# Kernel optimization log

Hardware: AMD Instinct MI355X
Metric: run time of the kernel (lower is better)

The kernel has to match this reference:

```python
import jax, jax.numpy as jnp
import numpy as np

B, T, C, H = 1, 4096, 768, 12
D = C // H  # 64


def setup_inputs() -> dict:
    key = jax.random.key(0)
    k1, k2, k3, k4, k5 = jax.random.split(key, 5)
    x = jax.random.normal(k1, (B, T, C), dtype=jnp.float32)
    # causal mask: 1.0 where attention is DISALLOWED (strict upper triangle)
    mask = (1.0 - jnp.tril(jnp.ones((T, T), dtype=jnp.float32)))[None, None, :, :]
    s_attn = 1.0 / np.sqrt(C)
    W_qkv = jax.random.normal(k2, (C, 3 * C), dtype=jnp.float32) * s_attn
    b_qkv = jnp.zeros((3 * C,), dtype=jnp.float32)
    W_proj = jax.random.normal(k3, (C, C), dtype=jnp.float32) * s_attn
    b_proj = jnp.zeros((C,), dtype=jnp.float32)
    return {"x": x, "mask": mask, "W_qkv": W_qkv, "b_qkv": b_qkv,
            "W_proj": W_proj, "b_proj": b_proj}


def reference(x, mask, W_qkv, b_qkv, W_proj, b_proj):
    qkv = jnp.einsum('btc,cf->btf', x, W_qkv) + b_qkv        # [B,T,3C]
    q, k, v = jnp.split(qkv, 3, axis=2)
    # [B,T,C] -> [B,H,T,D]
    q = q.reshape(B, T, H, D).transpose(0, 2, 1, 3)
    k = k.reshape(B, T, H, D).transpose(0, 2, 1, 3)
    v = v.reshape(B, T, H, D).transpose(0, 2, 1, 3)
    att = jnp.einsum('bhqd,bhkd->bhqk', q, k) * (1.0 / jnp.sqrt(jnp.float32(D)))
    att = att + mask * (-1e9)
    att = jax.nn.softmax(att, axis=-1)                        # [B,H,T,T]
    y = jnp.einsum('bhqk,bhkd->bhqd', att, v)                 # [B,H,T,D]
    y = y.transpose(0, 2, 1, 3).reshape(B, T, C)
    return jnp.einsum('btc,cf->btf', y, W_proj) + b_proj
```

## Files before the change

kernel.cpp:

```cpp
#include <hip/hip_runtime.h>
#include <hip/hip_bf16.h>

typedef unsigned short u16t;
typedef short bf16x8 __attribute__((ext_vector_type(8)));
typedef short bf16x4 __attribute__((ext_vector_type(4)));
typedef float f32x4 __attribute__((ext_vector_type(4)));

#define T_SEQ 4096
#define NH    12
#define HD    64
#define C3    2304
#define CDIM  768
#define STRIP_KV 512
#define SLOTS 144
#define SC_F  0.18033688011112042f

__device__ __forceinline__ float bf2f(u16t u) {
  union { unsigned int i; float f; } c; c.i = ((unsigned int)u) << 16; return c.f;
}
__device__ __forceinline__ u16t f2bf(float f) {
  union { float f; unsigned int i; } c; c.f = f;
  unsigned int u = c.i;
  u += 0x7fffu + ((u >> 16) & 1u);
  return (u16t)(u >> 16);
}
__device__ __forceinline__ unsigned pk2bf(float a, float b) {
  __hip_bfloat162 h = __float22bfloat162_rn(make_float2(a, b));
  union { __hip_bfloat162 h; unsigned u; } c; c.h = h; return c.u;
}
__device__ __forceinline__ void gload16(const u16t* g, u16t* l) {
  __builtin_amdgcn_global_load_lds((const __attribute__((address_space(1))) void*)g,
                                   (__attribute__((address_space(3))) void*)l,
                                   16, 0, 0);
}

#define BARRIER_LGKM() __asm__ __volatile__("s_waitcnt lgkmcnt(0)\n\ts_barrier" ::: "memory")

__global__ __launch_bounds__(256) void convert_to_bf16(const float* __restrict__ in,
                                                       u16t* __restrict__ out, int n) {
  int i = blockIdx.x * 256 + threadIdx.x;
  const int stride = gridDim.x * 256;
  for (; i < n; i += stride) out[i] = f2bf(in[i]);
}

__global__ __launch_bounds__(256) void transpose_weights(const float* __restrict__ Wqkv,
                                                         const float* __restrict__ Wproj,
                                                         u16t* __restrict__ WqkvT,
                                                         u16t* __restrict__ WprojT) {
  __shared__ u16t tile[32][33];
  const int z = blockIdx.z;
  const int Cc = z ? CDIM : C3;
  if (z && blockIdx.x >= (unsigned)(CDIM / 32)) return;
  const float* in = z ? Wproj : Wqkv;
  u16t* out = z ? WprojT : WqkvT;
  const int tx = threadIdx.x, ty = threadIdx.y;
  const int c0 = blockIdx.x * 32, r0 = blockIdx.y * 32;
#pragma unroll
  for (int i = 0; i < 32; i += 8)
    tile[ty + i][tx] = f2bf(in[(size_t)(r0 + ty + i) * Cc + c0 + tx]);
  __syncthreads();
#pragma unroll
  for (int i = 0; i < 32; i += 8)
    out[(size_t)(c0 + ty + i) * CDIM + r0 + tx] = tile[tx][ty + i];
}

template <int MT, int NF, bool OUTF32>
__global__ __launch_bounds__(256) void gemm_bt_bias(
    const u16t* __restrict__ A, const u16t* __restrict__ Bt,
    const float* __restrict__ bias, void* __restrict__ Cout,
    int M, int N, int K, int qcols, float qscale) {
  constexpr int BN = 32 * NF;
  constexpr int MI = MT / 32;
  __shared__ u16t lA[2][MT * 32];
  __shared__ u16t lB[2][BN * 32];
  const int t = threadIdx.x;
  const int lane = t & 63;
  const int wid  = t >> 6;
  const int quad = lane >> 4, l16 = lane & 15;
  const int m0 = blockIdx.y * MT, n0 = blockIdx.x * BN;
  const int wm = (wid >> 1) * (16 * MI), wn = (wid & 1) * (16 * NF);

  f32x4 acc[MI][NF];
#pragma unroll
  for (int i = 0; i < MI; ++i)
#pragma unroll
    for (int j = 0; j < NF; ++j) acc[i][j] = (f32x4){0.f, 0.f, 0.f, 0.f};

  for (int k0 = 0; k0 < K; k0 += 64) {
#pragma unroll
    for (int half = 0; half < 2; ++half) {
      const int kk = k0 + half * 32;
#pragma unroll
      for (int rd = 0; rd < MT / 64; ++rd) {
        const int e = rd * 256 + t;
        gload16(A + (size_t)(m0 + (e >> 2)) * K + kk + (e & 3) * 8, &lA[half][e * 8]);
      }
#pragma unroll
      for (int rd = 0; rd < NF / 2; ++rd) {
        const int e = rd * 256 + t;
        gload16(Bt + (size_t)(n0 + (e >> 2)) * K + kk + (e & 3) * 8, &lB[half][e * 8]);
      }
    }
    __syncthreads();
#pragma unroll
    for (int half = 0; half < 2; ++half) {
      bf16x8 af[MI], bfr[NF];
#pragma unroll
      for (int i = 0; i < MI; ++i)
        af[i] = *(const bf16x8*)&lA[half][(wm + i * 16 + l16) * 32 + quad * 8];
#pragma unroll
      for (int i = 0; i < NF; ++i)
        bfr[i] = *(const bf16x8*)&lB[half][(wn + i * 16 + l16) * 32 + quad * 8];
#pragma unroll
      for (int i = 0; i < MI; ++i)
#pragma unroll
        for (int j = 0; j < NF; ++j)
          acc[i][j] = __builtin_amdgcn_mfma_f32_16x16x32_bf16(af[i], bfr[j], acc[i][j], 0, 0, 0);
    }
    __syncthreads();
  }

#pragma unroll
  for (int j = 0; j < NF; ++j) {
    const int col = n0 + wn + j * 16 + l16;
    const float bv = bias[col];
    const float cs = (col < qcols) ? qscale : 1.0f;
#pragma unroll
    for (int i = 0; i < MI; ++i) {
      const int rowb = m0 + wm + i * 16 + quad * 4;
#pragma unroll
      for (int r = 0; r < 4; ++r) {
        const float val = (acc[i][j][r] + bv) * cs;
        const size_t idx = (size_t)(rowb + r) * N + col;
        if (OUTF32) ((float*)Cout)[idx] = val;
        else        ((u16t*)Cout)[idx] = f2bf(val);
      }
    }
  }
}

#define KSTR 88
#define VSTR 88

__global__ __launch_bounds__(256, 4) void attn_partial(const u16t* __restrict__ qkv,
                                                       u16t* __restrict__ pO,
                                                       float* __restrict__ pL) {
  const int h     = blockIdx.x;
  const int strip = blockIdx.y;
  const int qt    = 31 - (int)blockIdx.z;
  const int q0 = qt * 128;
  const int kv_begin = strip * STRIP_KV;
  const int kv_end   = q0 + 128;
  if (kv_begin >= kv_end) return;
  const int kv_stop = (kv_begin + STRIP_KV < kv_end) ? kv_begin + STRIP_KV : kv_end;
  const int a = qt >> 2, b = qt & 3;
  const int slot = (a + 1) * (2 * a + b) + strip;

  __shared__ u16t lK[64 * KSTR];
  __shared__ u16t lVt[64 * VSTR];

  const int t = threadIdx.x;
  const int lane = t & 63;
  const int wid  = t >> 6;
  const int quad = lane >> 4, l16 = lane & 15;
  const int wr = q0 + wid * 32;

  const int krow = t >> 3, kcol = (t & 7) * 8;
  const int vk0 = 4 * (t >> 4);
  const int vd0 = 4 * (t & 15);
  const int vswz = (t & 3) << 3;
  const u16t* Kbase = qkv + CDIM + h * HD;
  const u16t* Vbase = qkv + 2 * CDIM + h * HD;

  bf16x8 qf[2][2];
#pragma unroll
  for (int qn = 0; qn < 2; ++qn) {
    const int row = wr + qn * 16 + l16;
#pragma unroll
    for (int kd = 0; kd < 2; ++kd)
      qf[qn][kd] = *(const bf16x8*)(qkv + (size_t)row * C3 + h * HD + kd * 32 + quad * 8);
  }

  f32x4 oaccT[4][2];
  f32x4 laccT[2];
#pragma unroll
  for (int dn = 0; dn < 4; ++dn)
#pragma unroll
    for (int qn = 0; qn < 2; ++qn) oaccT[dn][qn] = (f32x4){0.f, 0.f, 0.f, 0.f};
#pragma unroll
  for (int qn = 0; qn < 2; ++qn) laccT[qn] = (f32x4){0.f, 0.f, 0.f, 0.f};
  bf16x4 ones4;
#pragma unroll
  for (int i = 0; i < 4; ++i) ones4[i] = (short)0x3F80;

  const int pswz = ((l16 >> 2) & 3) << 3;

  uint4 kreg0, kreg1;
  union { uint2 u; u16t hw[4]; } vreg[4];

#define LOAD_TILE(KV0)                                                        \
  do {                                                                        \
    kreg0 = *(const uint4*)(Kbase + (size_t)((KV0) + krow) * C3 + kcol);      \
    kreg1 = *(const uint4*)(Kbase + (size_t)((KV0) + krow + 32) * C3 + kcol); \
    _Pragma("unroll")                                                         \
    for (int i = 0; i < 4; ++i)                                               \
      vreg[i].u = *(const uint2*)(Vbase + (size_t)((KV0) + vk0 + i) * C3 + vd0); \
  } while (0)

#define STORE_TILE()                                                          \
  do {                                                                        \
    *(uint4*)&lK[krow * KSTR + kcol] = kreg0;                                 \
    *(uint4*)&lK[(krow + 32) * KSTR + kcol] = kreg1;                          \
    _Pragma("unroll")                                                         \
    for (int j = 0; j < 4; ++j) {                                             \
      union { uint2 u; u16t hw[4]; } w;                                       \
      w.hw[0] = vreg[0].hw[j]; w.hw[1] = vreg[1].hw[j];                       \
      w.hw[2] = vreg[2].hw[j]; w.hw[3] = vreg[3].hw[j];                       \
      *(uint2*)&lVt[(vd0 + j) * VSTR + (vk0 ^ vswz)] = w.u;                   \
    }                                                                         \
  } while (0)

  LOAD_TILE(kv_begin);
  STORE_TILE();

  for (int kv0 = kv_begin; kv0 < kv_stop; kv0 += 64) {
    const bool havenext = (kv0 + 64 < kv_stop);
    if (havenext) LOAD_TILE(kv0 + 64);
    BARRIER_LGKM();

    if (kv0 <= wr + 31) {
      f32x4 sacc[4][2];
#pragma unroll
      for (int kvt = 0; kvt < 4; ++kvt) {
        bf16x8 kf0 = *(const bf16x8*)&lK[(kvt * 16 + l16) * KSTR + quad * 8];
        bf16x8 kf1 = *(const bf16x8*)&lK[(kvt * 16 + l16) * KSTR + 32 + quad * 8];
#pragma unroll
        for (int qn = 0; qn < 2; ++qn) {
          f32x4 s = (f32x4){0.f, 0.f, 0.f, 0.f};
          s = __builtin_amdgcn_mfma_f32_16x16x32_bf16(kf0, qf[qn][0], s, 0, 0, 0);
          s = __builtin_amdgcn_mfma_f32_16x16x32_bf16(kf1, qf[qn][1], s, 0, 0, 0);
          sacc[kvt][qn] = s;
        }
      }
      const bool need_mask = (kv0 + 63 > wr);
      bf16x4 pbf[4][2];
#pragma unroll
      for (int kvt = 0; kvt < 4; ++kvt)
#pragma unroll
        for (int qn = 0; qn < 2; ++qn) {
          const int qg = wr + qn * 16 + l16;
          float pv[4];
#pragma unroll
          for (int r = 0; r < 4; ++r) {
            const int kvg = kv0 + kvt * 16 + quad * 4 + r;
            float p = __builtin_amdgcn_exp2f(sacc[kvt][qn][r]);
            if (need_mask && (kvg > qg)) p = 0.f;
            pv[r] = p;
          }
          union { bf16x4 v; unsigned u[2]; } pw;
          pw.u[0] = pk2bf(pv[0], pv[1]);
          pw.u[1] = pk2bf(pv[2], pv[3]);
          pbf[kvt][qn] = pw.v;
        }
#pragma unroll
      for (int kvt = 0; kvt < 4; ++kvt) {
        const int kvcol = (kvt * 16 + quad * 4) ^ pswz;
#pragma unroll
        for (int qn = 0; qn < 2; ++qn)
          laccT[qn] = __builtin_amdgcn_mfma_f32_16x16x16bf16_1k(
              ones4, pbf[kvt][qn], laccT[qn], 0, 0, 0);
#pragma unroll
        for (int dn = 0; dn < 4; ++dn) {
          bf16x4 vf = *(const bf16x4*)&lVt[(dn * 16 + l16) * VSTR + kvcol];
#pragma unroll
          for (int qn = 0; qn < 2; ++qn)
            oaccT[dn][qn] = __builtin_amdgcn_mfma_f32_16x16x16bf16_1k(
                vf, pbf[kvt][qn], oaccT[dn][qn], 0, 0, 0);
        }
      }
    }
    BARRIER_LGKM();
    if (havenext) STORE_TILE();
  }

  {
    u16t* scr = &lVt[wid * 16 * 80];
    u16t* po = pO + ((size_t)h * SLOTS + slot) * 128 * HD;
    float* pl = pL + ((size_t)h * SLOTS + slot) * 128;
#pragma unroll
    for (int qn = 0; qn < 2; ++qn) {
#pragma unroll
      for (int dn = 0; dn < 4; ++dn) {
        union { bf16x4 v; unsigned u[2]; } w;
        w.u[0] = pk2bf(oaccT[dn][qn][0], oaccT[dn][qn][1]);
        w.u[1] = pk2bf(oaccT[dn][qn][2], oaccT[dn][qn][3]);
        *(bf16x4*)&scr[l16 * 80 + dn * 16 + quad * 4] = w.v;
      }
      __asm__ __volatile__("s_waitcnt lgkmcnt(0)" ::: "memory");
      const int ql = wid * 32 + qn * 16 + l16;
      uint4 w0 = *(const uint4*)&scr[l16 * 80 + quad * 16];
      uint4 w1 = *(const uint4*)&scr[l16 * 80 + quad * 16 + 8];
      u16t* dst = po + (size_t)ql * HD + quad * 16;
      *(uint4*)dst = w0;
      *(uint4*)(dst + 8) = w1;
      if (quad == 0) pl[ql] = laccT[qn][0];
      __asm__ __volatile__("s_waitcnt lgkmcnt(0)" ::: "memory");
    }
  }
#undef LOAD_TILE
#undef STORE_TILE
}

__global__ __launch_bounds__(256) void attn_normalize(const u16t* __restrict__ pO,
                                                      const float* __restrict__ pL,
                                                      u16t* __restrict__ y) {
  const int i = blockIdx.x * 256 + threadIdx.x;
  const int q = i / (CDIM / 8), c8 = (i % (CDIM / 8)) * 8;
  const int h = c8 >> 6, d = c8 & 63;
  const int qt = q >> 7, ql = q & 127;
  const int a = qt >> 2, b = qt & 3;
  const int base = (a + 1) * (2 * a + b);
  const int ns = a + 1;
  float o[8] = {0.f, 0.f, 0.f, 0.f, 0.f, 0.f, 0.f, 0.f};
  float l = 0.f;
  for (int s = 0; s < ns; ++s) {
    const size_t sl = (size_t)h * SLOTS + base + s;
    union { uint4 u; u16t hw[8]; } v;
    v.u = *(const uint4*)&pO[(sl * 128 + ql) * HD + d];
#pragma unroll
    for (int j = 0; j < 8; ++j) o[j] += bf2f(v.hw[j]);
    l += pL[sl * 128 + ql];
  }
  const float rl = 1.0f / l;
  union { uint4 u; unsigned w[4]; } wv;
#pragma unroll
  for (int j = 0; j < 4; ++j)
    wv.w[j] = pk2bf(o[2 * j] * rl, o[2 * j + 1] * rl);
  *(uint4*)&y[(size_t)q * CDIM + c8] = wv.u;
}

extern "C" void kernel_launch(void* const* d_in, const int* in_sizes, int n_in,
                              void* d_out, int out_size, void* d_ws, size_t ws_size,
                              hipStream_t stream) {
  const float* x     = (const float*)d_in[0];
  const float* Wqkv  = (const float*)d_in[2];
  const float* bqkv  = (const float*)d_in[3];
  const float* Wproj = (const float*)d_in[4];
  const float* bproj = (const float*)d_in[5];

  u16t* qkv    = (u16t*)d_ws;
  u16t* ybuf   = qkv    + (size_t)T_SEQ * C3;
  u16t* WqkvT  = ybuf   + (size_t)T_SEQ * CDIM;
  u16t* WprojT = WqkvT  + (size_t)C3 * CDIM;
  u16t* pO     = WprojT + (size_t)CDIM * CDIM;
  float* pL    = (float*)(pO + (size_t)NH * SLOTS * 128 * HD);

  convert_to_bf16<<<1024, 256, 0, stream>>>(x, ybuf, T_SEQ * CDIM);
  transpose_weights<<<dim3(C3 / 32, CDIM / 32, 2), dim3(32, 8), 0, stream>>>(
      Wqkv, Wproj, WqkvT, WprojT);
  gemm_bt_bias<128, 4, false><<<dim3(C3 / 128, T_SEQ / 128), 256, 0, stream>>>(
      ybuf, WqkvT, bqkv, qkv, T_SEQ, C3, CDIM, CDIM, SC_F);
  attn_partial<<<dim3(NH, 8, T_SEQ / 128), 256, 0, stream>>>(qkv, pO, pL);
  attn_normalize<<<(T_SEQ * CDIM / 8) / 256, 256, 0, stream>>>(pO, pL, ybuf);
  gemm_bt_bias<128, 2, true><<<dim3(CDIM / 64, T_SEQ / 128), 256, 0, stream>>>(
      ybuf, WprojT, bproj, d_out, T_SEQ, CDIM, CDIM, 0, 1.0f);
}
```

Baseline: 232.1 us.

## Double-buffer GEMM k-loop, remap workgroups across XCDs, vectorize bf16 convert

The GEMM main loop now prefetches the next 32-wide k slice into the alternate LDS buffer while computing on the current one, replacing a load-all-then-compute step that left loads and MFMAs serialized. Block IDs are remapped so consecutive tiles land on the same XCD for better L2 reuse. The input fp32-to-bf16 conversion is vectorized to handle 8 elements per thread with 128-bit loads and stores. The pipeline halves the k step, which means more barriers per k, and the remap only applies when the workgroup count is divisible by 8.

```diff
diff --git a/kernel.cpp b/kernel.cpp
--- a/kernel.cpp
+++ b/kernel.cpp
@@ -37,10 +37,17 @@
 #define BARRIER_LGKM() __asm__ __volatile__("s_waitcnt lgkmcnt(0)\n\ts_barrier" ::: "memory")
 
 __global__ __launch_bounds__(256) void convert_to_bf16(const float* __restrict__ in,
-                                                       u16t* __restrict__ out, int n) {
+                                                       u16t* __restrict__ out, int n8) {
   int i = blockIdx.x * 256 + threadIdx.x;
   const int stride = gridDim.x * 256;
-  for (; i < n; i += stride) out[i] = f2bf(in[i]);
+  for (; i < n8; i += stride) {
+    const float4 a = ((const float4*)in)[2 * i];
+    const float4 b = ((const float4*)in)[2 * i + 1];
+    union { uint4 u; unsigned w[4]; } o;
+    o.w[0] = pk2bf(a.x, a.y); o.w[1] = pk2bf(a.z, a.w);
+    o.w[2] = pk2bf(b.x, b.y); o.w[3] = pk2bf(b.z, b.w);
+    ((uint4*)out)[i] = o.u;
+  }
 }
 
 __global__ __launch_bounds__(256) void transpose_weights(const float* __restrict__ Wqkv,
@@ -77,7 +84,13 @@
   const int lane = t & 63;
   const int wid  = t >> 6;
   const int quad = lane >> 4, l16 = lane & 15;
-  const int m0 = blockIdx.y * MT, n0 = blockIdx.x * BN;
+
+  const int gx = gridDim.x;
+  const int nwg = gx * (int)gridDim.y;
+  int bid = (int)blockIdx.y * gx + (int)blockIdx.x;
+  if ((nwg & 7) == 0) bid = (bid & 7) * (nwg >> 3) + (bid >> 3);
+  const int m0 = (bid / gx) * MT, n0 = (bid % gx) * BN;
+
   const int wm = (wid >> 1) * (16 * MI), wn = (wid & 1) * (16 * NF);
 
   f32x4 acc[MI][NF];
@@ -86,39 +99,43 @@
 #pragma unroll
     for (int j = 0; j < NF; ++j) acc[i][j] = (f32x4){0.f, 0.f, 0.f, 0.f};
 
-  for (int k0 = 0; k0 < K; k0 += 64) {
-#pragma unroll
-    for (int half = 0; half < 2; ++half) {
-      const int kk = k0 + half * 32;
-#pragma unroll
-      for (int rd = 0; rd < MT / 64; ++rd) {
-        const int e = rd * 256 + t;
-        gload16(A + (size_t)(m0 + (e >> 2)) * K + kk + (e & 3) * 8, &lA[half][e * 8]);
-      }
-#pragma unroll
-      for (int rd = 0; rd < NF / 2; ++rd) {
-        const int e = rd * 256 + t;
-        gload16(Bt + (size_t)(n0 + (e >> 2)) * K + kk + (e & 3) * 8, &lB[half][e * 8]);
-      }
-    }
+  auto stage = [&](int b, int k0) {
+#pragma unroll
+    for (int rd = 0; rd < MT / 64; ++rd) {
+      const int e = rd * 256 + t;
+      gload16(A + (size_t)(m0 + (e >> 2)) * K + k0 + (e & 3) * 8, &lA[b][e * 8]);
+    }
+#pragma unroll
+    for (int rd = 0; rd < NF / 2; ++rd) {
+      const int e = rd * 256 + t;
+      gload16(Bt + (size_t)(n0 + (e >> 2)) * K + k0 + (e & 3) * 8, &lB[b][e * 8]);
+    }
+  };
+  auto compute = [&](int b) {
+    bf16x8 af[MI], bfr[NF];
+#pragma unroll
+    for (int i = 0; i < MI; ++i)
+      af[i] = *(const bf16x8*)&lA[b][(wm + i * 16 + l16) * 32 + quad * 8];
+#pragma unroll
+    for (int i = 0; i < NF; ++i)
+      bfr[i] = *(const bf16x8*)&lB[b][(wn + i * 16 + l16) * 32 + quad * 8];
+#pragma unroll
+    for (int i = 0; i < MI; ++i)
+#pragma unroll
+      for (int j = 0; j < NF; ++j)
+        acc[i][j] = __builtin_amdgcn_mfma_f32_16x16x32_bf16(af[i], bfr[j], acc[i][j], 0, 0, 0);
+  };
+
+  stage(0, 0);
+  __syncthreads();
+  int cur = 0;
+  for (int k0 = 32; k0 < K; k0 += 32) {
+    stage(cur ^ 1, k0);
+    compute(cur);
     __syncthreads();
-#pragma unroll
-    for (int half = 0; half < 2; ++half) {
-      bf16x8 af[MI], bfr[NF];
-#pragma unroll
-      for (int i = 0; i < MI; ++i)
-        af[i] = *(const bf16x8*)&lA[half][(wm + i * 16 + l16) * 32 + quad * 8];
-#pragma unroll
-      for (int i = 0; i < NF; ++i)
-        bfr[i] = *(const bf16x8*)&lB[half][(wn + i * 16 + l16) * 32 + quad * 8];
-#pragma unroll
-      for (int i = 0; i < MI; ++i)
-#pragma unroll
-        for (int j = 0; j < NF; ++j)
-          acc[i][j] = __builtin_amdgcn_mfma_f32_16x16x32_bf16(af[i], bfr[j], acc[i][j], 0, 0, 0);
-    }
-    __syncthreads();
-  }
+    cur ^= 1;
+  }
+  compute(cur);
 
 #pragma unroll
   for (int j = 0; j < NF; ++j) {
@@ -355,7 +372,7 @@
   u16t* pO     = WprojT + (size_t)CDIM * CDIM;
   float* pL    = (float*)(pO + (size_t)NH * SLOTS * 128 * HD);
 
-  convert_to_bf16<<<1024, 256, 0, stream>>>(x, ybuf, T_SEQ * CDIM);
+  convert_to_bf16<<<1536, 256, 0, stream>>>(x, ybuf, T_SEQ * CDIM / 8);
   transpose_weights<<<dim3(C3 / 32, CDIM / 32, 2), dim3(32, 8), 0, stream>>>(
       Wqkv, Wproj, WqkvT, WprojT);
   gemm_bt_bias<128, 4, false><<<dim3(C3 / 128, T_SEQ / 128), 256, 0, stream>>>(
```

New measurement: 223.7 us. 3.6% less time.
